# Optimization experiments

Measured on AMD Instinct MI355X. Metric: run time of the kernel, lower is better.

The kernel has to match this reference:

```python
import jax, jax.numpy as jnp
import numpy as np

B, N, C, OUT, K2 = 64, 4096, 64, 64, 4  # batch, lattice sites, in/out features, kersize^2

def setup_inputs() -> dict:
    key = jax.random.key(0)
    k1, k2, k3, k4 = jax.random.split(key, 4)
    std = 0.5 / jnp.sqrt(K2 * (C + OUT))  # matches module's init stddev (W_scale=b_scale=1)
    x = jax.random.normal(k1, (B, N, C), dtype=jnp.float32)
    W = jax.random.normal(k2, (K2, C, OUT), dtype=jnp.float32) * std
    b = jax.random.normal(k3, (OUT,), dtype=jnp.float32) * std
    kernel2 = jax.random.randint(k4, (N, K2), 0, N, dtype=jnp.int32)
    return {"x": x, "W": W, "b": b, "kernel2": kernel2}

def reference(x, W, b, kernel2):
    # gather neighbors: [B, N, K2, C]; contract (K2, C) with W -> [B, N, OUT]
    y = jnp.einsum('bnkc,kco->bno', x[:, kernel2, :], W)
    # bias broadcast (original used tensordot with ones([B,N]))
    return y + b
```

## Files before the change

### kernel.cpp

```cpp
#include <hip/hip_runtime.h>
#include <stdint.h>


#define N_SITES  4096
#define C_DIM    64
#define OUT_DIM  64

typedef __attribute__((ext_vector_type(8))) short bf16x8;
typedef __attribute__((ext_vector_type(4))) float f32x4;

__device__ __forceinline__ uint32_t pack2_bf16(float f0, float f1) {
    uint32_t u0 = __float_as_uint(f0) + 0x8000u;
    uint32_t u1 = __float_as_uint(f1) + 0x8000u;
    return __builtin_amdgcn_perm(u1, u0, 0x07060302u);
}

template<int N> __device__ __forceinline__ void wait_vmcnt() {
    asm volatile("s_waitcnt vmcnt(%0)" :: "n"(N) : "memory");
}

__device__ __forceinline__ void gll16(const float* p, uint32_t m0v) {
    asm volatile("s_mov_b32 m0, %1\n\t"
                 "global_load_lds_dwordx4 %0, off"
                 :: "v"(p), "s"(m0v) : "memory");
}

__global__ __launch_bounds__(64, 1)
void conv_async_kernel(const float* __restrict__ x, const float* __restrict__ W,
                       const float* __restrict__ bias, const int* __restrict__ kernel2,
                       float* __restrict__ out)
{
    __shared__ __align__(1024) uint8_t lds_raw[33280];

    const int lane = threadIdx.x;
    const int bi   = blockIdx.x;
    const int half = bi >> 10;
    const int r    = bi & 1023;
    const int bgl  = r & 7;
    const int sg   = r >> 3;
    const int bg   = bgl + half * 8;
    const int n0   = sg * 32;
    const int b0   = bg * 4;

    const int c  = lane & 15;
    const int q  = lane >> 4;
    const int sl = c >> 2;
    const int bb = c & 3;

    const int g  = lane >> 4;
    const int u  = lane & 15;

    if (lane < 32) {
        int4 iv = ((const int4*)kernel2)[n0 + lane];
        *(int4*)(lds_raw + 32768 + lane * 16) = iv;
    }

    bf16x8 aw[4][8];
    #pragma unroll
    for (int t = 0; t < 4; ++t)
        #pragma unroll
        for (int s = 0; s < 8; ++s) {
            uint32_t* ap = (uint32_t*)&aw[t][s];
            #pragma unroll
            for (int uu = 0; uu < 4; ++uu) {
                float f0 = W[(size_t)(s*32 + q*8 + 2*uu    ) * OUT_DIM + t*16 + c];
                float f1 = W[(size_t)(s*32 + q*8 + 2*uu + 1) * OUT_DIM + t*16 + c];
                ap[uu] = pack2_bf16(f0, f1);
            }
        }

    f32x4 bias_r[4];
    #pragma unroll
    for (int t = 0; t < 4; ++t) bias_r[t] = *(const f32x4*)&bias[t*16 + q*4];

    const float* gxn = x + (size_t)(b0 + g) * (N_SITES * C_DIM)
                     + (size_t)((((u >> 1) ^ g) * 8) + (u & 1) * 4);

    const uint32_t lds0 =
        __builtin_amdgcn_readfirstlane((uint32_t)(uintptr_t)lds_raw);

    wait_vmcnt<0>();

    auto issue_ht = [&](int i) {
        const int pp = i >> 1, h = i & 1;
        const int* ibase = (const int*)(lds_raw + 32768 + pp * 64);
        const uint32_t m0s = lds0 + (uint32_t)(i & 3) * 8192;
        #pragma unroll
        for (int kl = 0; kl < 2; ++kl) {
            #pragma unroll
            for (int slp = 0; slp < 4; ++slp) {
                const int nk = ibase[slp * 4 + 2 * h + kl];
                const float* row = gxn + (size_t)(uint32_t)nk * C_DIM;
                gll16(row, m0s + (uint32_t)kl * 4096 + (uint32_t)slp * 1024);
            }
        }
    };

    auto comp_ht = [&](int i, f32x4* acc) {
        const uint32_t tb = (uint32_t)(i & 3) * 8192;
        const int hb = (i & 1) * 4;
        #pragma unroll
        for (int kl = 0; kl < 2; ++kl)
        #pragma unroll
        for (int hs = 0; hs < 2; ++hs) {
            const uint8_t* pb = lds_raw + tb + (uint32_t)kl * 4096
                              + (uint32_t)c * 256
                              + (uint32_t)((((hs * 4 + q) ^ (c & 3)) * 32));
            f32x4 xa = *(const f32x4*)(pb);
            f32x4 xb = *(const f32x4*)(pb + 16);
            bf16x8 bf;
            uint32_t* bp = (uint32_t*)&bf;
            bp[0] = pack2_bf16(xa[0], xa[1]);
            bp[1] = pack2_bf16(xa[2], xa[3]);
            bp[2] = pack2_bf16(xb[0], xb[1]);
            bp[3] = pack2_bf16(xb[2], xb[3]);
            #pragma unroll
            for (int t = 0; t < 4; ++t)
                acc[t] = __builtin_amdgcn_mfma_f32_16x16x32_bf16(
                    aw[t][hb + kl * 2 + hs], bf, acc[t], 0, 0, 0);
        }
    };

    issue_ht(0);
    issue_ht(1);
    issue_ht(2);
    issue_ht(3);

    #pragma unroll
    for (int p = 0; p < 8; ++p) {
        f32x4 acc[4];
        #pragma unroll
        for (int t = 0; t < 4; ++t) acc[t] = (f32x4){0.f, 0.f, 0.f, 0.f};

        if      (p == 0) wait_vmcnt<24>();
        else if (p == 1) wait_vmcnt<28>();
        else if (p == 7) wait_vmcnt<16>();
        else             wait_vmcnt<32>();
        comp_ht(2*p, acc);
        if (p <= 5) issue_ht(2*p + 4);

        if      (p == 0) wait_vmcnt<24>();
        else if (p == 1) wait_vmcnt<28>();
        else if (p == 6) wait_vmcnt<24>();
        else if (p == 7) wait_vmcnt<8>();
        else             wait_vmcnt<32>();
        comp_ht(2*p + 1, acc);
        if (p <= 5) issue_ht(2*p + 5);

        const int n = n0 + p*4 + sl;
        float* op = out + ((size_t)(b0 + bb) * N_SITES + n) * OUT_DIM + q*4;
        #pragma unroll
        for (int t = 0; t < 4; ++t)
            *(f32x4*)(op + t*16) = acc[t] + bias_r[t];
    }
}

extern "C" void kernel_launch(void* const* d_in, const int* in_sizes, int n_in,
                              void* d_out, int out_size, void* d_ws, size_t ws_size,
                              hipStream_t stream) {
    const float* x       = (const float*)d_in[0];
    const float* W       = (const float*)d_in[1];
    const float* bias    = (const float*)d_in[2];
    const int*   kernel2 = (const int*)d_in[3];
    float* out = (float*)d_out;

    conv_async_kernel<<<2048, 64, 0, stream>>>(x, W, bias, kernel2, out);
}
```

Before: 137.0 us.

## Precast x to bf16 in workspace before gathering, halving gather traffic

```diff
diff --git a/kernel.cpp b/kernel.cpp
--- a/kernel.cpp
+++ b/kernel.cpp
@@ -19,18 +19,39 @@
     asm volatile("s_waitcnt vmcnt(%0)" :: "n"(N) : "memory");
 }
 
-__device__ __forceinline__ void gll16(const float* p, uint32_t m0v) {
+__device__ __forceinline__ void gll16(const void* p, uint32_t m0v) {
     asm volatile("s_mov_b32 m0, %1\n\t"
                  "global_load_lds_dwordx4 %0, off"
                  :: "v"(p), "s"(m0v) : "memory");
 }
 
+__global__ __launch_bounds__(256, 1)
+void precast_kernel(const float* __restrict__ x, uint32_t* __restrict__ xb)
+{
+    const uint32_t n8 = 64u * 4096u * 64u / 8u;
+    for (uint32_t i = blockIdx.x * 256 + threadIdx.x; i < n8;
+         i += gridDim.x * 256) {
+        const f32x4* p = (const f32x4*)x + 2 * (size_t)i;
+        f32x4 a = p[0], b = p[1];
+        uint4 o;
+        o.x = pack2_bf16(a[0], a[1]); o.y = pack2_bf16(a[2], a[3]);
+        o.z = pack2_bf16(b[0], b[1]); o.w = pack2_bf16(b[2], b[3]);
+        ((uint4*)xb)[i] = o;
+    }
+}
+
+__host__ __device__ constexpr int wait_for(int i) {
+    return (i <= 1) ? 8 : (i == 2 || i == 3) ? 12
+         : (i == 15) ? 4 : (i == 14) ? 12
+         : (i & 1) ? 12 : 16;
+}
+
 __global__ __launch_bounds__(64, 1)
-void conv_async_kernel(const float* __restrict__ x, const float* __restrict__ W,
-                       const float* __restrict__ bias, const int* __restrict__ kernel2,
-                       float* __restrict__ out)
+void conv_bf16_kernel(const uint8_t* __restrict__ xb, const float* __restrict__ W,
+                      const float* __restrict__ bias, const int* __restrict__ kernel2,
+                      float* __restrict__ out)
 {
-    __shared__ __align__(1024) uint8_t lds_raw[33280];
+    __shared__ __align__(1024) uint8_t lds_raw[12800];
 
     const int lane = threadIdx.x;
     const int bi   = blockIdx.x;
@@ -47,6 +68,132 @@
     const int sl = c >> 2;
     const int bb = c & 3;
 
+    const int hq = lane >> 3;
+    const int lm = lane & 7;
+
+    if (lane < 32)
+        ((int4*)(lds_raw + 12288))[lane] = ((const int4*)kernel2)[n0 + lane];
+    const int* lds_idx = (const int*)(lds_raw + 12288);
+
+    bf16x8 aw[4][8];
+    #pragma unroll
+    for (int t = 0; t < 4; ++t)
+        #pragma unroll
+        for (int s = 0; s < 8; ++s) {
+            uint32_t* ap = (uint32_t*)&aw[t][s];
+            #pragma unroll
+            for (int u = 0; u < 4; ++u) {
+                float f0 = W[(size_t)(s*32 + q*8 + 2*u    ) * OUT_DIM + t*16 + c];
+                float f1 = W[(size_t)(s*32 + q*8 + 2*u + 1) * OUT_DIM + t*16 + c];
+                ap[u] = pack2_bf16(f0, f1);
+            }
+        }
+
+    f32x4 bias_r[4];
+    #pragma unroll
+    for (int t = 0; t < 4; ++t) bias_r[t] = *(const f32x4*)&bias[t*16 + q*4];
+
+    const uint8_t* gsrc = xb + (size_t)(b0 + (hq >> 1)) * (N_SITES * 128)
+                        + (size_t)((lm ^ hq) * 16);
+
+    const uint32_t lds0 =
+        __builtin_amdgcn_readfirstlane((uint32_t)(uintptr_t)lds_raw);
+
+    wait_vmcnt<0>();
+    __builtin_amdgcn_sched_barrier(0);
+
+    auto issue = [&](int i) {
+        const int h = i & 1, pp = i >> 1;
+        const int* ib = lds_idx + pp * 16;
+        const uint32_t m0s = lds0 + (uint32_t)(i % 3) * 4096;
+        #pragma unroll
+        for (int j = 0; j < 4; ++j) {
+            const int tap = 2 * h + (j >> 1);
+            const int sp  = (j & 1) * 2;
+            const int nk0 = ib[(sp    ) * 4 + tap];
+            const int nk1 = ib[(sp + 1) * 4 + tap];
+            const int nk  = (hq & 1) ? nk1 : nk0;
+            gll16(gsrc + (size_t)(uint32_t)nk * 128,
+                  m0s + (uint32_t)j * 1024);
+        }
+    };
+
+    auto comp = [&](int i, f32x4* acc) {
+        const uint32_t tb = (uint32_t)(i % 3) * 4096;
+        const int h = i & 1;
+        const uint32_t rr = (uint32_t)(bb * 2 + (sl & 1));
+        #pragma unroll
+        for (int tl = 0; tl < 2; ++tl) {
+            const uint32_t js = (uint32_t)(tl * 2 + (sl >> 1));
+            #pragma unroll
+            for (int hs = 0; hs < 2; ++hs) {
+                const uint32_t uw = ((uint32_t)(hs * 4 + q)) ^ rr;
+                const bf16x8 bf = *(const bf16x8*)(lds_raw + tb + js * 1024
+                                                   + rr * 128 + uw * 16);
+                #pragma unroll
+                for (int t = 0; t < 4; ++t)
+                    acc[t] = __builtin_amdgcn_mfma_f32_16x16x32_bf16(
+                        aw[t][h*4 + tl*2 + hs], bf, acc[t], 0, 0, 0);
+            }
+        }
+    };
+
+    auto dostore = [&](int p, const f32x4* acc) {
+        const int n = n0 + p * 4 + sl;
+        float* op = out + ((size_t)(b0 + bb) * N_SITES + n) * OUT_DIM + q * 4;
+        #pragma unroll
+        for (int t = 0; t < 4; ++t)
+            *(f32x4*)(op + t*16) = acc[t] + bias_r[t];
+    };
+
+    issue(0);
+    issue(1);
+    issue(2);
+
+    f32x4 acc[4];
+
+    #define STEP(i)                                                           \
+    {                                                                         \
+        wait_vmcnt<wait_for(i)>();                                            \
+        __builtin_amdgcn_sched_barrier(0);                                    \
+        if (((i) & 1) == 0) {                                                 \
+            acc[0] = (f32x4){0.f,0.f,0.f,0.f};                                \
+            acc[1] = (f32x4){0.f,0.f,0.f,0.f};                                \
+            acc[2] = (f32x4){0.f,0.f,0.f,0.f};                                \
+            acc[3] = (f32x4){0.f,0.f,0.f,0.f};                                \
+        }                                                                     \
+        comp((i), acc);                                                       \
+        if ((i) <= 12) issue((i) + 3);                                        \
+        if ((i) & 1) dostore((i) >> 1, acc);                                  \
+    }
+
+    STEP(0);  STEP(1);  STEP(2);  STEP(3);
+    STEP(4);  STEP(5);  STEP(6);  STEP(7);
+    STEP(8);  STEP(9);  STEP(10); STEP(11);
+    STEP(12); STEP(13); STEP(14); STEP(15);
+
+    #undef STEP
+}
+
+__global__ __launch_bounds__(64, 1)
+void conv_f32_kernel(const float* __restrict__ x, const float* __restrict__ W,
+                     const float* __restrict__ bias, const int* __restrict__ kernel2,
+                     float* __restrict__ out)
+{
+    __shared__ __align__(1024) uint8_t lds_raw[33280];
+    const int lane = threadIdx.x;
+    const int bi   = blockIdx.x;
+    const int half = bi >> 10;
+    const int r    = bi & 1023;
+    const int bgl  = r & 7;
+    const int sg   = r >> 3;
+    const int bg   = bgl + half * 8;
+    const int n0   = sg * 32;
+    const int b0   = bg * 4;
+    const int c  = lane & 15;
+    const int q  = lane >> 4;
+    const int sl = c >> 2;
+    const int bb = c & 3;
     const int g  = lane >> 4;
     const int u  = lane & 15;
 
@@ -75,7 +222,6 @@
 
     const float* gxn = x + (size_t)(b0 + g) * (N_SITES * C_DIM)
                      + (size_t)((((u >> 1) ^ g) * 8) + (u & 1) * 4);
-
     const uint32_t lds0 =
         __builtin_amdgcn_readfirstlane((uint32_t)(uintptr_t)lds_raw);
 
@@ -86,14 +232,13 @@
         const int* ibase = (const int*)(lds_raw + 32768 + pp * 64);
         const uint32_t m0s = lds0 + (uint32_t)(i & 3) * 8192;
         #pragma unroll
-        for (int kl = 0; kl < 2; ++kl) {
+        for (int kl = 0; kl < 2; ++kl)
             #pragma unroll
             for (int slp = 0; slp < 4; ++slp) {
                 const int nk = ibase[slp * 4 + 2 * h + kl];
-                const float* row = gxn + (size_t)(uint32_t)nk * C_DIM;
-                gll16(row, m0s + (uint32_t)kl * 4096 + (uint32_t)slp * 1024);
+                gll16(gxn + (size_t)(uint32_t)nk * C_DIM,
+                      m0s + (uint32_t)kl * 4096 + (uint32_t)slp * 1024);
             }
-        }
     };
 
     auto comp_ht = [&](int i, f32x4* acc) {
@@ -121,10 +266,7 @@
         }
     };
 
-    issue_ht(0);
-    issue_ht(1);
-    issue_ht(2);
-    issue_ht(3);
+    issue_ht(0); issue_ht(1); issue_ht(2); issue_ht(3);
 
     #pragma unroll
     for (int p = 0; p < 8; ++p) {
@@ -164,5 +306,12 @@
     const int*   kernel2 = (const int*)d_in[3];
     float* out = (float*)d_out;
 
-    conv_async_kernel<<<2048, 64, 0, stream>>>(x, W, bias, kernel2, out);
-}
+    const size_t need = (size_t)64 * 4096 * 64 * 2;
+    if (ws_size >= need && d_ws != nullptr) {
+        precast_kernel<<<2048, 256, 0, stream>>>(x, (uint32_t*)d_ws);
+        conv_bf16_kernel<<<2048, 64, 0, stream>>>((const uint8_t*)d_ws, W,
+                                                  bias, kernel2, out);
+    } else {
+        conv_f32_kernel<<<2048, 64, 0, stream>>>(x, W, bias, kernel2, out);
+    }
+}
```

New measurement: 134.6 us. About the same (-1.8%).
